# Kernel tuning notes

Hardware: AMD Instinct MI355X
Metric: run time of the kernel (lower is better)

Reference implementation:

```python
import jax, jax.numpy as jnp
import numpy as np

NUM_SLOTS = 128
HIDDEN_DIM = 4096
EMA_ALPHA = 0.1
WRITE_TOP_K = 2048
T_TOKENS = 8192
K_RET = 4
BATCH_IDX = 0


def setup_inputs() -> dict:
    key = jax.random.key(0)
    k1, k2, k3, k4, k5 = jax.random.split(key, 5)
    hidden_states = jax.random.normal(k1, (T_TOKENS, HIDDEN_DIM), dtype=jnp.float32)
    # attention weights over K retrieved slots: normalized to a distribution per token
    raw = jax.random.uniform(k2, (T_TOKENS, K_RET), dtype=jnp.float32)
    attention_weights = raw / raw.sum(axis=-1, keepdims=True)
    slot_indices = jax.random.randint(k3, (T_TOKENS, K_RET), 0, NUM_SLOTS)
    memory = jax.random.normal(k4, (1, NUM_SLOTS, HIDDEN_DIM), dtype=jnp.float32)
    W_imp = jax.random.normal(k5, (1, HIDDEN_DIM), dtype=jnp.float32) * 0.02
    b_imp = jnp.zeros((1,), dtype=jnp.float32)
    return {
        "hidden_states": hidden_states,
        "attention_weights": attention_weights,
        "slot_indices": slot_indices,
        "memory": memory,
        "W_imp": W_imp,
        "b_imp": b_imp,
    }


def _compute_importance(hidden_states, attention_weights, W_imp, b_imp):
    # magnitude: ||h_t||_2, [T]
    magnitude = jnp.linalg.norm(hidden_states, axis=-1)
    # attention surprise: normalized entropy over K slots, [T]
    attn = attention_weights
    entropy = -(attn * jnp.log(attn + 1e-8)).sum(axis=-1)
    max_entropy = jnp.log(jnp.asarray(attn.shape[-1], dtype=jnp.float32))
    surprise = entropy / jnp.maximum(max_entropy, 1e-8)
    importance = magnitude * (1.0 + surprise)  # 'combined' mode
    learned_score = hidden_states @ W_imp[0] + b_imp[0]  # [T]
    return importance + jax.nn.sigmoid(learned_score)


def reference(hidden_states, attention_weights, slot_indices, memory, W_imp, b_imp):
    # importance-based top-K token selection
    importance = _compute_importance(hidden_states, attention_weights, W_imp, b_imp)
    _, topk_idx = jax.lax.top_k(importance, WRITE_TOP_K)
    h_sel = hidden_states[topk_idx]          # [Ksel, D]
    si_sel = slot_indices[topk_idx]          # [Ksel, K]

    # membership[t, n] = 1 if slot n appears anywhere in token t's retrieved slots
    # (matches torch's (slot_indices == idx).any(dim=-1))
    onehot = jax.nn.one_hot(si_sel, NUM_SLOTS, dtype=jnp.float32)  # [Ksel, K, N]
    member = (onehot.sum(axis=1) > 0).astype(jnp.float32)          # [Ksel, N]

    counts = member.sum(axis=0)                                    # [N]
    sums = jnp.einsum("tn,td->nd", member, h_sel)                  # [N, D]
    agg = sums / jnp.maximum(counts, 1.0)[:, None]                 # segment mean

    current = memory[BATCH_IDX]                                    # [N, D]
    updated = EMA_ALPHA * agg + (1.0 - EMA_ALPHA) * current
    new_slots = jnp.where(counts[:, None] > 0, updated, current)
    return memory.at[BATCH_IDX].set(new_slots)
```

## Files before the change

### kernel.cpp

```cpp
#include <hip/hip_runtime.h>
#include <math.h>

#define T_TOK 8192
#define HDIM 4096
#define NSLOT 128
#define KRET 4
#define TOPK 2048
#define ALPHA 0.1f
#define MAXC 2048

__global__ __launch_bounds__(256) void importance_kernel(
    const float* __restrict__ h, const float* __restrict__ attn,
    const float* __restrict__ W, const float* __restrict__ b,
    float* __restrict__ imp, int* __restrict__ rank)
{
    const int wid  = threadIdx.x >> 6;
    const int lane = threadIdx.x & 63;
    const int t = blockIdx.x * 4 + wid;
    const float4* hv = reinterpret_cast<const float4*>(h + (size_t)t * HDIM);
    const float4* Wv = reinterpret_cast<const float4*>(W);
    float sumsq = 0.f, dot = 0.f;
    #pragma unroll 4
    for (int i = 0; i < 16; i++) {
        float4 x = hv[lane + i * 64];
        float4 w = Wv[lane + i * 64];
        sumsq += x.x * x.x + x.y * x.y + x.z * x.z + x.w * x.w;
        dot   += x.x * w.x + x.y * w.y + x.z * w.z + x.w * w.w;
    }
    #pragma unroll
    for (int off = 32; off > 0; off >>= 1) {
        sumsq += __shfl_down(sumsq, off);
        dot   += __shfl_down(dot, off);
    }
    if (lane == 0) {
        float mag = sqrtf(sumsq);
        float ent = 0.f;
        #pragma unroll
        for (int k = 0; k < KRET; k++) {
            float a = attn[t * KRET + k];
            ent -= a * logf(a + 1e-8f);
        }
        float surprise = ent / logf(4.0f);
        float score = dot + b[0];
        float sig = 1.0f / (1.0f + expf(-score));
        imp[t] = mag * (1.0f + surprise) + sig;
        rank[t] = 0;
    }
}

__global__ __launch_bounds__(256) void rank_kernel(
    const float* __restrict__ imp, int* __restrict__ rank)
{
    const int cb = blockIdx.x & 31;
    const int sl = blockIdx.x >> 5;
    __shared__ float tile[256];
    const int base = sl * 256;
    tile[threadIdx.x] = imp[base + threadIdx.x];
    __syncthreads();
    const int t = cb * 256 + threadIdx.x;
    const float mine = imp[t];
    int r = 0;
    #pragma unroll 8
    for (int i = 0; i < 256; i++) {
        float v = tile[i];
        int s = base + i;
        r += (v > mine) || (v == mine && s < t);
    }
    if (r) atomicAdd(&rank[t], r);
}

__global__ __launch_bounds__(256) void slotlist_kernel(
    const int* __restrict__ rank, const int* __restrict__ si,
    int* __restrict__ lists, int* __restrict__ counts)
{
    const int slot = blockIdx.x;
    const int tid = threadIdx.x;
    __shared__ int part[256];
    const int base = tid * 32;
    unsigned mask = 0;
    int local = 0;
    const int4* si4 = reinterpret_cast<const int4*>(si);
    #pragma unroll 8
    for (int j = 0; j < 32; j++) {
        const int t = base + j;
        int4 s = si4[t];
        bool sel = rank[t] < TOPK;
        bool mem = (s.x == slot) | (s.y == slot) | (s.z == slot) | (s.w == slot);
        if (sel && mem) { mask |= (1u << j); local++; }
    }
    part[tid] = local;
    __syncthreads();
    for (int off = 1; off < 256; off <<= 1) {
        int v = part[tid];
        int add = (tid >= off) ? part[tid - off] : 0;
        __syncthreads();
        part[tid] = v + add;
        __syncthreads();
    }
    int pos = part[tid] - local;
    int* mylist = lists + (size_t)slot * MAXC;
    for (int j = 0; j < 32; j++) {
        if (mask & (1u << j)) mylist[pos++] = base + j;
    }
    if (tid == 255) counts[slot] = part[255];
}

__global__ __launch_bounds__(256) void update_kernel(
    const float* __restrict__ h, const float* __restrict__ mem,
    const int* __restrict__ lists, const int* __restrict__ counts,
    float* __restrict__ out)
{
    const int slot = blockIdx.x >> 2;
    const int chunk = blockIdx.x & 3;
    const int cnt = counts[slot];
    __shared__ int s_list[MAXC];
    for (int i = threadIdx.x; i < cnt; i += 256)
        s_list[i] = lists[(size_t)slot * MAXC + i];
    __syncthreads();

    const int dbase = chunk * 1024 + threadIdx.x * 4;
    float4 acc = make_float4(0.f, 0.f, 0.f, 0.f);
    int i = 0;
    for (; i + 4 <= cnt; i += 4) {
        int t0 = s_list[i], t1 = s_list[i + 1];
        int t2 = s_list[i + 2], t3 = s_list[i + 3];
        float4 x0 = *reinterpret_cast<const float4*>(h + (size_t)t0 * HDIM + dbase);
        float4 x1 = *reinterpret_cast<const float4*>(h + (size_t)t1 * HDIM + dbase);
        float4 x2 = *reinterpret_cast<const float4*>(h + (size_t)t2 * HDIM + dbase);
        float4 x3 = *reinterpret_cast<const float4*>(h + (size_t)t3 * HDIM + dbase);
        acc.x += x0.x + x1.x + x2.x + x3.x;
        acc.y += x0.y + x1.y + x2.y + x3.y;
        acc.z += x0.z + x1.z + x2.z + x3.z;
        acc.w += x0.w + x1.w + x2.w + x3.w;
    }
    for (; i < cnt; i++) {
        int t0 = s_list[i];
        float4 x0 = *reinterpret_cast<const float4*>(h + (size_t)t0 * HDIM + dbase);
        acc.x += x0.x; acc.y += x0.y; acc.z += x0.z; acc.w += x0.w;
    }

    const size_t o = (size_t)slot * HDIM + dbase;
    float4 cur = *reinterpret_cast<const float4*>(mem + o);
    float4 r;
    if (cnt > 0) {
        float inv = 1.0f / (float)cnt;
        r.x = ALPHA * (acc.x * inv) + (1.f - ALPHA) * cur.x;
        r.y = ALPHA * (acc.y * inv) + (1.f - ALPHA) * cur.y;
        r.z = ALPHA * (acc.z * inv) + (1.f - ALPHA) * cur.z;
        r.w = ALPHA * (acc.w * inv) + (1.f - ALPHA) * cur.w;
    } else {
        r = cur;
    }
    *reinterpret_cast<float4*>(out + o) = r;
}

extern "C" void kernel_launch(void* const* d_in, const int* in_sizes, int n_in,
                              void* d_out, int out_size, void* d_ws, size_t ws_size,
                              hipStream_t stream) {
    const float* h    = (const float*)d_in[0];
    const float* attn = (const float*)d_in[1];
    const int*   si   = (const int*)d_in[2];
    const float* mem  = (const float*)d_in[3];
    const float* W    = (const float*)d_in[4];
    const float* b    = (const float*)d_in[5];
    float* out = (float*)d_out;

    char* ws = (char*)d_ws;
    float* imp    = (float*)(ws);
    int*   rank   = (int*)(ws + 32768);
    int*   counts = (int*)(ws + 65536);
    int*   lists  = (int*)(ws + 131072);

    importance_kernel<<<T_TOK / 4, 256, 0, stream>>>(h, attn, W, b, imp, rank);
    rank_kernel<<<1024, 256, 0, stream>>>(imp, rank);
    slotlist_kernel<<<NSLOT, 256, 0, stream>>>(rank, si, lists, counts);
    update_kernel<<<NSLOT * 4, 256, 0, stream>>>(h, mem, lists, counts, out);
}
```

Baseline: 59.90 us.

## Replace per-slot gather-sum with bf16 MFMA membership-matrix einsum

Replaces the per-slot token-list build and gather-sum with a gather kernel that compacts the selected tokens into a bf16 matrix and writes a dense transposed bf16 membership matrix. An MFMA bf16 einsum kernel then computes the slot sums and applies the EMA update in its epilogue. This avoids re-reading each token's fp32 row once per slot it belongs to, but converts the hidden states to bf16 and so loses precision. Count zeroing is folded into the rank kernel, and each gather block rescans rank to find its prefix offset.

```diff
diff --git a/kernel.cpp b/kernel.cpp
--- a/kernel.cpp
+++ b/kernel.cpp
@@ -6,8 +6,16 @@
 #define NSLOT 128
 #define KRET 4
 #define TOPK 2048
-#define ALPHA 0.1f
-#define MAXC 2048
+#define KSEL 2048
+
+typedef __attribute__((ext_vector_type(8))) short short8v;
+typedef __attribute__((ext_vector_type(4))) float floatx4;
+
+__device__ __forceinline__ ushort f2bf(float f) {
+    unsigned u = __float_as_uint(f);
+    unsigned r = (u + 0x7FFFu + ((u >> 16) & 1u)) >> 16;
+    return (ushort)r;
+}
 
 __global__ __launch_bounds__(256) void importance_kernel(
     const float* __restrict__ h, const float* __restrict__ attn,
@@ -49,8 +57,10 @@
 }
 
 __global__ __launch_bounds__(256) void rank_kernel(
-    const float* __restrict__ imp, int* __restrict__ rank)
-{
+    const float* __restrict__ imp, int* __restrict__ rank,
+    int* __restrict__ counts)
+{
+    if (blockIdx.x == 0 && threadIdx.x < NSLOT) counts[threadIdx.x] = 0;
     const int cb = blockIdx.x & 31;
     const int sl = blockIdx.x >> 5;
     __shared__ float tile[256];
@@ -69,89 +79,128 @@
     if (r) atomicAdd(&rank[t], r);
 }
 
-__global__ __launch_bounds__(256) void slotlist_kernel(
-    const int* __restrict__ rank, const int* __restrict__ si,
-    int* __restrict__ lists, int* __restrict__ counts)
-{
-    const int slot = blockIdx.x;
+__global__ __launch_bounds__(256) void gather_kernel(
+    const float* __restrict__ h, const int* __restrict__ rank,
+    const int* __restrict__ si, ushort* __restrict__ Hsel,
+    ushort* __restrict__ M_T, int* __restrict__ counts)
+{
+    const int bid = blockIdx.x;
     const int tid = threadIdx.x;
-    __shared__ int part[256];
-    const int base = tid * 32;
-    unsigned mask = 0;
-    int local = 0;
-    const int4* si4 = reinterpret_cast<const int4*>(si);
-    #pragma unroll 8
-    for (int j = 0; j < 32; j++) {
-        const int t = base + j;
-        int4 s = si4[t];
-        bool sel = rank[t] < TOPK;
-        bool mem = (s.x == slot) | (s.y == slot) | (s.z == slot) | (s.w == slot);
-        if (sel && mem) { mask |= (1u << j); local++; }
-    }
-    part[tid] = local;
-    __syncthreads();
-    for (int off = 1; off < 256; off <<= 1) {
-        int v = part[tid];
-        int add = (tid >= off) ? part[tid - off] : 0;
+    const int t0 = bid * 32;
+
+    __shared__ int s_red[4];
+    __shared__ int s_flag[32], s_pos[32], s_tok[32];
+    __shared__ int s_base, s_n;
+
+    int c = 0;
+    for (int t = tid; t < t0; t += 256) c += (rank[t] < TOPK) ? 1 : 0;
+    #pragma unroll
+    for (int off = 32; off > 0; off >>= 1) c += __shfl_down(c, off);
+    if ((tid & 63) == 0) s_red[tid >> 6] = c;
+    if (tid < 32) s_flag[tid] = (rank[t0 + tid] < TOPK) ? 1 : 0;
+    __syncthreads();
+    if (tid == 0) {
+        s_base = s_red[0] + s_red[1] + s_red[2] + s_red[3];
+        int p = 0;
+        for (int j = 0; j < 32; j++) { s_pos[j] = p; p += s_flag[j]; }
+        s_n = p;
+    }
+    __syncthreads();
+    const int n = s_n, base = s_base;
+    if (tid < 32 && s_flag[tid]) s_tok[s_pos[tid]] = t0 + tid;
+    __syncthreads();
+
+    for (int i = tid; i < NSLOT * n; i += 256) {
+        int srow = i / n;
+        int ci = i - srow * n;
+        M_T[(size_t)srow * KSEL + base + ci] = 0;
+    }
+
+    for (int i = 0; i < n; i++) {
+        const int t = s_tok[i];
+        const float4* src = reinterpret_cast<const float4*>(h + (size_t)t * HDIM) + tid * 4;
+        ushort us[16];
+        #pragma unroll
+        for (int q = 0; q < 4; q++) {
+            float4 x = src[q];
+            us[q * 4 + 0] = f2bf(x.x); us[q * 4 + 1] = f2bf(x.y);
+            us[q * 4 + 2] = f2bf(x.z); us[q * 4 + 3] = f2bf(x.w);
+        }
+        uint4* dst = reinterpret_cast<uint4*>(Hsel + (size_t)(base + i) * HDIM) + tid * 2;
+        dst[0] = *reinterpret_cast<const uint4*>(&us[0]);
+        dst[1] = *reinterpret_cast<const uint4*>(&us[8]);
+    }
+    __syncthreads();
+
+    if (tid < 32 && s_flag[tid]) {
+        const int p = base + s_pos[tid];
+        int4 s4 = reinterpret_cast<const int4*>(si)[t0 + tid];
+        bool dy = (s4.y != s4.x);
+        bool dz = (s4.z != s4.x) && (s4.z != s4.y);
+        bool dw = (s4.w != s4.x) && (s4.w != s4.y) && (s4.w != s4.z);
+        const ushort ONE = 0x3F80;
+        M_T[(size_t)s4.x * KSEL + p] = ONE; atomicAdd(&counts[s4.x], 1);
+        if (dy) { M_T[(size_t)s4.y * KSEL + p] = ONE; atomicAdd(&counts[s4.y], 1); }
+        if (dz) { M_T[(size_t)s4.z * KSEL + p] = ONE; atomicAdd(&counts[s4.z], 1); }
+        if (dw) { M_T[(size_t)s4.w * KSEL + p] = ONE; atomicAdd(&counts[s4.w], 1); }
+    }
+}
+
+__global__ __launch_bounds__(256) void einsum_kernel(
+    const ushort* __restrict__ Hsel, const ushort* __restrict__ M_T,
+    const int* __restrict__ counts, const float* __restrict__ mem,
+    float* __restrict__ out)
+{
+    const int bid = blockIdx.x;
+    const int sg = bid >> 7;
+    const int db = bid & 127;
+    const int tid = threadIdx.x;
+    const int w = tid >> 6, l = tid & 63;
+    const int stile = sg * 64 + w * 16;
+    const int lrow = l & 15, lgrp = l >> 4;
+
+    __shared__ __align__(16) ushort Hlds[32][40];
+
+    floatx4 acc0 = {0.f, 0.f, 0.f, 0.f};
+    floatx4 acc1 = {0.f, 0.f, 0.f, 0.f};
+
+    const int r = tid >> 3;
+    const int cc = (tid & 7) * 4;
+
+    for (int kk = 0; kk < KSEL; kk += 32) {
+        uint2 v = *reinterpret_cast<const uint2*>(
+            Hsel + (size_t)(kk + r) * HDIM + db * 32 + cc);
+        Hlds[cc + 0][r] = (ushort)(v.x & 0xFFFFu);
+        Hlds[cc + 1][r] = (ushort)(v.x >> 16);
+        Hlds[cc + 2][r] = (ushort)(v.y & 0xFFFFu);
+        Hlds[cc + 3][r] = (ushort)(v.y >> 16);
         __syncthreads();
-        part[tid] = v + add;
+
+        short8v a = *reinterpret_cast<const short8v*>(
+            M_T + (size_t)(stile + lrow) * KSEL + kk + 8 * lgrp);
+        short8v b0 = *reinterpret_cast<const short8v*>(&Hlds[lrow][8 * lgrp]);
+        short8v b1 = *reinterpret_cast<const short8v*>(&Hlds[16 + lrow][8 * lgrp]);
+        acc0 = __builtin_amdgcn_mfma_f32_16x16x32_bf16(a, b0, acc0, 0, 0, 0);
+        acc1 = __builtin_amdgcn_mfma_f32_16x16x32_bf16(a, b1, acc1, 0, 0, 0);
         __syncthreads();
     }
-    int pos = part[tid] - local;
-    int* mylist = lists + (size_t)slot * MAXC;
-    for (int j = 0; j < 32; j++) {
-        if (mask & (1u << j)) mylist[pos++] = base + j;
-    }
-    if (tid == 255) counts[slot] = part[255];
-}
-
-__global__ __launch_bounds__(256) void update_kernel(
-    const float* __restrict__ h, const float* __restrict__ mem,
-    const int* __restrict__ lists, const int* __restrict__ counts,
-    float* __restrict__ out)
-{
-    const int slot = blockIdx.x >> 2;
-    const int chunk = blockIdx.x & 3;
-    const int cnt = counts[slot];
-    __shared__ int s_list[MAXC];
-    for (int i = threadIdx.x; i < cnt; i += 256)
-        s_list[i] = lists[(size_t)slot * MAXC + i];
-    __syncthreads();
-
-    const int dbase = chunk * 1024 + threadIdx.x * 4;
-    float4 acc = make_float4(0.f, 0.f, 0.f, 0.f);
-    int i = 0;
-    for (; i + 4 <= cnt; i += 4) {
-        int t0 = s_list[i], t1 = s_list[i + 1];
-        int t2 = s_list[i + 2], t3 = s_list[i + 3];
-        float4 x0 = *reinterpret_cast<const float4*>(h + (size_t)t0 * HDIM + dbase);
-        float4 x1 = *reinterpret_cast<const float4*>(h + (size_t)t1 * HDIM + dbase);
-        float4 x2 = *reinterpret_cast<const float4*>(h + (size_t)t2 * HDIM + dbase);
-        float4 x3 = *reinterpret_cast<const float4*>(h + (size_t)t3 * HDIM + dbase);
-        acc.x += x0.x + x1.x + x2.x + x3.x;
-        acc.y += x0.y + x1.y + x2.y + x3.y;
-        acc.z += x0.z + x1.z + x2.z + x3.z;
-        acc.w += x0.w + x1.w + x2.w + x3.w;
-    }
-    for (; i < cnt; i++) {
-        int t0 = s_list[i];
-        float4 x0 = *reinterpret_cast<const float4*>(h + (size_t)t0 * HDIM + dbase);
-        acc.x += x0.x; acc.y += x0.y; acc.z += x0.z; acc.w += x0.w;
-    }
-
-    const size_t o = (size_t)slot * HDIM + dbase;
-    float4 cur = *reinterpret_cast<const float4*>(mem + o);
-    float4 r;
-    if (cnt > 0) {
-        float inv = 1.0f / (float)cnt;
-        r.x = ALPHA * (acc.x * inv) + (1.f - ALPHA) * cur.x;
-        r.y = ALPHA * (acc.y * inv) + (1.f - ALPHA) * cur.y;
-        r.z = ALPHA * (acc.z * inv) + (1.f - ALPHA) * cur.z;
-        r.w = ALPHA * (acc.w * inv) + (1.f - ALPHA) * cur.w;
-    } else {
-        r = cur;
-    }
-    *reinterpret_cast<float4*>(out + o) = r;
+
+    #pragma unroll
+    for (int reg = 0; reg < 4; reg++) {
+        const int slot = stile + lgrp * 4 + reg;
+        const int cnt = counts[slot];
+        const float inv = (cnt > 0) ? (1.0f / (float)cnt) : 0.f;
+        {
+            const size_t o = (size_t)slot * HDIM + db * 32 + lrow;
+            float cur = mem[o];
+            out[o] = (cnt > 0) ? (0.1f * (acc0[reg] * inv) + 0.9f * cur) : cur;
+        }
+        {
+            const size_t o = (size_t)slot * HDIM + db * 32 + 16 + lrow;
+            float cur = mem[o];
+            out[o] = (cnt > 0) ? (0.1f * (acc1[reg] * inv) + 0.9f * cur) : cur;
+        }
+    }
 }
 
 extern "C" void kernel_launch(void* const* d_in, const int* in_sizes, int n_in,
@@ -166,13 +215,14 @@
     float* out = (float*)d_out;
 
     char* ws = (char*)d_ws;
-    float* imp    = (float*)(ws);
-    int*   rank   = (int*)(ws + 32768);
-    int*   counts = (int*)(ws + 65536);
-    int*   lists  = (int*)(ws + 131072);
+    float*  imp    = (float*)(ws);
+    int*    rank   = (int*)(ws + 32768);
+    int*    counts = (int*)(ws + 65536);
+    ushort* M_T    = (ushort*)(ws + 131072);
+    ushort* Hsel   = (ushort*)(ws + 2097152);
 
     importance_kernel<<<T_TOK / 4, 256, 0, stream>>>(h, attn, W, b, imp, rank);
-    rank_kernel<<<1024, 256, 0, stream>>>(imp, rank);
-    slotlist_kernel<<<NSLOT, 256, 0, stream>>>(rank, si, lists, counts);
-    update_kernel<<<NSLOT * 4, 256, 0, stream>>>(h, mem, lists, counts, out);
-}
+    rank_kernel<<<1024, 256, 0, stream>>>(imp, rank, counts);
+    gather_kernel<<<256, 256, 0, stream>>>(h, rank, si, Hsel, M_T, counts);
+    einsum_kernel<<<256, 256, 0, stream>>>(Hsel, M_T, counts, mem, out);
+}
```

New measurement: 108.1 us. +80.5%, slower.

## Gather FP8-quantized hidden states and fuse slot-list building into update kernel

Applied to the files above, without the earlier changes.

The importance pass now also writes an FP8 (e4m3) copy of every hidden-state row. The update kernel gathers from that compact copy instead of the fp32 rows, cutting the bytes read per gathered element by four. The separate slot-list kernel is removed: each update block builds its slot's member list itself using wavefront ballots, which saves one launch and the global list round-trip. The cost is an extra full-size FP8 write during the importance pass, repeated scans of rank and slot indices by every update block, and a loss of accuracy in the segment means from FP8 rounding.

```diff
diff --git a/kernel.cpp b/kernel.cpp
--- a/kernel.cpp
+++ b/kernel.cpp
@@ -7,18 +7,81 @@
 #define KRET 4
 #define TOPK 2048
 #define ALPHA 0.1f
-#define MAXC 2048
+
+typedef unsigned char uchar;
+
+__device__ __forceinline__ uchar f2fp8_manual(float f) {
+    float a = fabsf(f);
+    unsigned s = (__float_as_uint(f) >> 24) & 0x80u;
+    if (a >= 448.f) return (uchar)(s | 0x7Eu);
+    if (a < 0.001953125f) {
+        int q = (int)(a * 512.f + 0.5f);
+        return (uchar)(s | (unsigned)q);
+    }
+    unsigned u = __float_as_uint(a);
+    int e = (int)((u >> 23) & 0xFF) - 127;
+    if (e < -6) {
+        int q = (int)(a * 512.f + 0.5f);
+        if (q >= 8) return (uchar)(s | 0x08u);
+        return (uchar)(s | (unsigned)q);
+    }
+    unsigned man = u & 0x7FFFFFu;
+    unsigned keep = man >> 20;
+    unsigned rem = man & 0xFFFFFu;
+    if (rem > 0x80000u || (rem == 0x80000u && (keep & 1u))) {
+        keep++;
+        if (keep == 8u) { keep = 0u; e++; }
+    }
+    if (e > 8 || (e == 8 && keep > 6u)) return (uchar)(s | 0x7Eu);
+    return (uchar)(s | ((unsigned)(e + 7) << 3) | keep);
+}
+
+__device__ __forceinline__ unsigned f32x4_to_fp8(float4 x) {
+#if __has_builtin(__builtin_amdgcn_cvt_pk_fp8_f32)
+    int w = 0;
+    w = __builtin_amdgcn_cvt_pk_fp8_f32(x.x, x.y, w, false);
+    w = __builtin_amdgcn_cvt_pk_fp8_f32(x.z, x.w, w, true);
+    return (unsigned)w;
+#else
+    return (unsigned)f2fp8_manual(x.x) | ((unsigned)f2fp8_manual(x.y) << 8) |
+           ((unsigned)f2fp8_manual(x.z) << 16) | ((unsigned)f2fp8_manual(x.w) << 24);
+#endif
+}
+
+__device__ __forceinline__ float fp8tof_manual(uchar b) {
+    unsigned E = (b >> 3) & 0xFu;
+    unsigned m = b & 7u;
+    float v = (E == 0) ? (float)m * 0.001953125f
+                       : __uint_as_float(((E + 120u) << 23) | (m << 20));
+    return (b & 0x80u) ? -v : v;
+}
+
+__device__ __forceinline__ void fp8x4_to_f32(unsigned w, float* o) {
+#if __has_builtin(__builtin_amdgcn_cvt_pk_f32_fp8)
+    typedef __attribute__((ext_vector_type(2))) float f32x2;
+    f32x2 lo = __builtin_amdgcn_cvt_pk_f32_fp8((int)w, false);
+    f32x2 hi = __builtin_amdgcn_cvt_pk_f32_fp8((int)w, true);
+    o[0] = lo.x; o[1] = lo.y; o[2] = hi.x; o[3] = hi.y;
+#else
+    o[0] = fp8tof_manual((uchar)(w & 0xFF));
+    o[1] = fp8tof_manual((uchar)((w >> 8) & 0xFF));
+    o[2] = fp8tof_manual((uchar)((w >> 16) & 0xFF));
+    o[3] = fp8tof_manual((uchar)((w >> 24) & 0xFF));
+#endif
+}
 
 __global__ __launch_bounds__(256) void importance_kernel(
     const float* __restrict__ h, const float* __restrict__ attn,
     const float* __restrict__ W, const float* __restrict__ b,
-    float* __restrict__ imp, int* __restrict__ rank)
+    float* __restrict__ imp, int* __restrict__ rank,
+    unsigned* __restrict__ h8)
 {
     const int wid  = threadIdx.x >> 6;
     const int lane = threadIdx.x & 63;
     const int t = blockIdx.x * 4 + wid;
     const float4* hv = reinterpret_cast<const float4*>(h + (size_t)t * HDIM);
     const float4* Wv = reinterpret_cast<const float4*>(W);
+    unsigned* h8row = h8 + (size_t)t * (HDIM / 4);
     float sumsq = 0.f, dot = 0.f;
     #pragma unroll 4
     for (int i = 0; i < 16; i++) {
@@ -26,6 +89,7 @@
         float4 w = Wv[lane + i * 64];
         sumsq += x.x * x.x + x.y * x.y + x.z * x.z + x.w * x.w;
         dot   += x.x * w.x + x.y * w.y + x.z * w.z + x.w * w.w;
+        h8row[lane + i * 64] = f32x4_to_fp8(x);
     }
     #pragma unroll
     for (int off = 32; off > 0; off >>= 1) {
@@ -69,77 +133,68 @@
     if (r) atomicAdd(&rank[t], r);
 }
 
-__global__ __launch_bounds__(256) void slotlist_kernel(
-    const int* __restrict__ rank, const int* __restrict__ si,
-    int* __restrict__ lists, int* __restrict__ counts)
-{
-    const int slot = blockIdx.x;
-    const int tid = threadIdx.x;
-    __shared__ int part[256];
-    const int base = tid * 32;
-    unsigned mask = 0;
-    int local = 0;
-    const int4* si4 = reinterpret_cast<const int4*>(si);
-    #pragma unroll 8
-    for (int j = 0; j < 32; j++) {
-        const int t = base + j;
-        int4 s = si4[t];
-        bool sel = rank[t] < TOPK;
-        bool mem = (s.x == slot) | (s.y == slot) | (s.z == slot) | (s.w == slot);
-        if (sel && mem) { mask |= (1u << j); local++; }
-    }
-    part[tid] = local;
-    __syncthreads();
-    for (int off = 1; off < 256; off <<= 1) {
-        int v = part[tid];
-        int add = (tid >= off) ? part[tid - off] : 0;
-        __syncthreads();
-        part[tid] = v + add;
-        __syncthreads();
-    }
-    int pos = part[tid] - local;
-    int* mylist = lists + (size_t)slot * MAXC;
-    for (int j = 0; j < 32; j++) {
-        if (mask & (1u << j)) mylist[pos++] = base + j;
-    }
-    if (tid == 255) counts[slot] = part[255];
-}
-
-__global__ __launch_bounds__(256) void update_kernel(
-    const float* __restrict__ h, const float* __restrict__ mem,
-    const int* __restrict__ lists, const int* __restrict__ counts,
+__global__ __launch_bounds__(256) void update_fp8_kernel(
+    const unsigned* __restrict__ h8, const int* __restrict__ rank,
+    const int* __restrict__ si, const float* __restrict__ mem,
     float* __restrict__ out)
 {
     const int slot = blockIdx.x >> 2;
     const int chunk = blockIdx.x & 3;
-    const int cnt = counts[slot];
-    __shared__ int s_list[MAXC];
-    for (int i = threadIdx.x; i < cnt; i += 256)
-        s_list[i] = lists[(size_t)slot * MAXC + i];
+    const int tid = threadIdx.x;
+    const int w = tid >> 6, lane = tid & 63;
+
+    __shared__ int s_list[4][2048];
+    __shared__ int s_wcnt[4];
+
+    const int4* si4 = reinterpret_cast<const int4*>(si);
+    int base = 0;
+    for (int it = 0; it < 32; it++) {
+        const int t = (w << 11) + (it << 6) + lane;
+        bool sel = rank[t] < TOPK;
+        int4 s = si4[t];
+        bool mem4 = (s.x == slot) | (s.y == slot) | (s.z == slot) | (s.w == slot);
+        bool m = sel && mem4;
+        unsigned long long bal = __ballot(m);
+        if (m) {
+            int pos = base + (int)__popcll(bal & ((1ull << lane) - 1ull));
+            s_list[w][pos] = t;
+        }
+        base += (int)__popcll(bal);
+    }
+    if (lane == 0) s_wcnt[w] = base;
     __syncthreads();
 
-    const int dbase = chunk * 1024 + threadIdx.x * 4;
+    const int cnt = s_wcnt[0] + s_wcnt[1] + s_wcnt[2] + s_wcnt[3];
+    const int dword = chunk * 256 + tid;
     float4 acc = make_float4(0.f, 0.f, 0.f, 0.f);
-    int i = 0;
-    for (; i + 4 <= cnt; i += 4) {
-        int t0 = s_list[i], t1 = s_list[i + 1];
-        int t2 = s_list[i + 2], t3 = s_list[i + 3];
-        float4 x0 = *reinterpret_cast<const float4*>(h + (size_t)t0 * HDIM + dbase);
-        float4 x1 = *reinterpret_cast<const float4*>(h + (size_t)t1 * HDIM + dbase);
-        float4 x2 = *reinterpret_cast<const float4*>(h + (size_t)t2 * HDIM + dbase);
-        float4 x3 = *reinterpret_cast<const float4*>(h + (size_t)t3 * HDIM + dbase);
-        acc.x += x0.x + x1.x + x2.x + x3.x;
-        acc.y += x0.y + x1.y + x2.y + x3.y;
-        acc.z += x0.z + x1.z + x2.z + x3.z;
-        acc.w += x0.w + x1.w + x2.w + x3.w;
-    }
-    for (; i < cnt; i++) {
-        int t0 = s_list[i];
-        float4 x0 = *reinterpret_cast<const float4*>(h + (size_t)t0 * HDIM + dbase);
-        acc.x += x0.x; acc.y += x0.y; acc.z += x0.z; acc.w += x0.w;
-    }
-
-    const size_t o = (size_t)slot * HDIM + dbase;
+    for (int wv = 0; wv < 4; wv++) {
+        const int n = s_wcnt[wv];
+        const int* lst = s_list[wv];
+        int i = 0;
+        for (; i + 4 <= n; i += 4) {
+            unsigned q0 = h8[(size_t)lst[i]     * (HDIM / 4) + dword];
+            unsigned q1 = h8[(size_t)lst[i + 1] * (HDIM / 4) + dword];
+            unsigned q2 = h8[(size_t)lst[i + 2] * (HDIM / 4) + dword];
+            unsigned q3 = h8[(size_t)lst[i + 3] * (HDIM / 4) + dword];
+            float v[4];
+            fp8x4_to_f32(q0, v);
+            acc.x += v[0]; acc.y += v[1]; acc.z += v[2]; acc.w += v[3];
+            fp8x4_to_f32(q1, v);
+            acc.x += v[0]; acc.y += v[1]; acc.z += v[2]; acc.w += v[3];
+            fp8x4_to_f32(q2, v);
+            acc.x += v[0]; acc.y += v[1]; acc.z += v[2]; acc.w += v[3];
+            fp8x4_to_f32(q3, v);
+            acc.x += v[0]; acc.y += v[1]; acc.z += v[2]; acc.w += v[3];
+        }
+        for (; i < n; i++) {
+            unsigned q0 = h8[(size_t)lst[i] * (HDIM / 4) + dword];
+            float v[4];
+            fp8x4_to_f32(q0, v);
+            acc.x += v[0]; acc.y += v[1]; acc.z += v[2]; acc.w += v[3];
+        }
+    }
+
+    const size_t o = (size_t)slot * HDIM + (size_t)dword * 4;
     float4 cur = *reinterpret_cast<const float4*>(mem + o);
     float4 r;
     if (cnt > 0) {
@@ -166,13 +221,11 @@
     float* out = (float*)d_out;
 
     char* ws = (char*)d_ws;
-    float* imp    = (float*)(ws);
-    int*   rank   = (int*)(ws + 32768);
-    int*   counts = (int*)(ws + 65536);
-    int*   lists  = (int*)(ws + 131072);
-
-    importance_kernel<<<T_TOK / 4, 256, 0, stream>>>(h, attn, W, b, imp, rank);
+    float*    imp  = (float*)(ws);
+    int*      rank = (int*)(ws + 32768);
+    unsigned* h8   = (unsigned*)(ws + 131072);
+
+    importance_kernel<<<T_TOK / 4, 256, 0, stream>>>(h, attn, W, b, imp, rank, h8);
     rank_kernel<<<1024, 256, 0, stream>>>(imp, rank);
-    slotlist_kernel<<<NSLOT, 256, 0, stream>>>(rank, si, lists, counts);
-    update_kernel<<<NSLOT * 4, 256, 0, stream>>>(h, mem, lists, counts, out);
-}
+    update_fp8_kernel<<<NSLOT * 4, 256, 0, stream>>>(h8, rank, si, mem, out);
+}
```

Result: slower. 63.55 us (+6.1%).
